# Optimization experiments

Hardware: AMD Instinct MI355X
Metric: run time of the kernel (lower is better)

## Reference

```python
import jax, jax.numpy as jnp
import numpy as np
import math

NEG = -1000000.0

def setup_inputs() -> dict:
    key = jax.random.key(0)
    k1, k2, k3, k4 = jax.random.split(key, 4)
    B, S, D = 64, 1024, 64
    query = jax.random.normal(k1, (B, S, D), dtype=jnp.float32)
    key_t = jax.random.normal(k2, (B, S, D), dtype=jnp.float32)
    value = jax.random.normal(k3, (B, S, D), dtype=jnp.float32)
    valid_lens = jax.random.randint(k4, (B,), 1, S + 1, dtype=jnp.int32)
    return {"query": query, "key": key_t, "value": value, "valid_lens": valid_lens}

def reference(query, key, value, valid_lens):
    # query/key/value: [B, S, D]; valid_lens: [B]
    d = query.shape[-1]
    scores = jnp.einsum('bqd,bkd->bqk', query, key) / math.sqrt(d)
    Sk = key.shape[1]
    # 1D valid_lens -> same mask for every query row (repeat_interleave semantics)
    mask = jnp.arange(Sk)[None, None, :] < valid_lens[:, None, None]  # [B,1,Sk]
    scores = jnp.where(mask, scores, NEG)
    weights = jax.nn.softmax(scores, axis=-1)
    # dropout p=0.0 -> identity
    return jnp.einsum('bqk,bkd->bqd', weights, value)
```

## Files before the change

### kernel.cpp

```cpp
#include <hip/hip_runtime.h>
#include <hip/hip_bf16.h>
#include <cstdint>


typedef __attribute__((ext_vector_type(8))) short short8;
typedef __attribute__((ext_vector_type(4))) short short4v;
typedef __attribute__((ext_vector_type(4))) float f32x4;

#define B_   64
#define S_   1024
#define D_   64
#define BQ   64
#define BK   64
#define KPAD 68

__device__ __forceinline__ uint32_t pk2(float a, float b) {
    float2 t; t.x = a; t.y = b;
    union { __hip_bfloat162 h; uint32_t u; } c;
    c.h = __float22bfloat162_rn(t);
    return c.u;
}
__device__ __forceinline__ unsigned short pbf(float f) {
    union { float f; uint32_t u; } v; v.f = f;
    return (unsigned short)((v.u + 0x8000u) >> 16);
}
__device__ __forceinline__ short8 ld8(const unsigned short* p) {
    short4v lo = *(const short4v*)p;
    short4v hi = *(const short4v*)(p + 4);
    return __builtin_shufflevector(lo, hi, 0, 1, 2, 3, 4, 5, 6, 7);
}

__global__ __launch_bounds__(256, 4)
void attn_fwd(const float* __restrict__ Q, const float* __restrict__ K,
              const float* __restrict__ V, const int* __restrict__ VL,
              float* __restrict__ Out) {
    __shared__ __align__(16) unsigned short lK [2][BK * KPAD];
    __shared__ __align__(16) unsigned short lVt[2][D_ * 64];
    __shared__ __align__(16) unsigned short lP [4 * 16 * KPAD];

    const int tid  = threadIdx.x;
    const int wave = tid >> 6;
    const int lane = tid & 63;
    const int col  = lane & 15;
    const int quad = lane >> 4;

    const int bid  = blockIdx.x;
    const int b    = (bid & 7) * 8 + (bid >> 7);
    const int q0   = ((bid >> 3) & 15) * BQ;
    const int vlen = VL[b];
    const int ntiles = (vlen + BK - 1) / BK;

    const int T  = tid >> 4;
    const int m  = tid & 15;
    const int Tl = T & 3;
    const int cb = T >> 2;
    const int dcs = m >> 1;
    const int sws = ((dcs & 1) << 2) | (dcs >> 1);

    const float* Kb = K + (size_t)b * S_ * D_ + 4 * m;
    const float* Vb = V + (size_t)b * S_ * D_ + 4 * m;

    float4 kr[4], vr[4];
    {
        #pragma unroll
        for (int j = 0; j < 4; ++j) {
            const int row = 2 * T + (j >> 1) * 32 + (j & 1);
            kr[j] = *(const float4*)(Kb + (size_t)row * D_);
            vr[j] = *(const float4*)(Vb + (size_t)row * D_);
        }
    }

    short8 qa[2];
    {
        const int qrow = q0 + wave * 16 + col;
        const float* qp = Q + ((size_t)b * S_ + qrow) * D_ + quad * 8;
        #pragma unroll
        for (int c = 0; c < 2; ++c) {
            float4 x0 = *(const float4*)(qp + c * 32);
            float4 x1 = *(const float4*)(qp + c * 32 + 4);
            union { uint32_t u[4]; short8 s; } qq;
            qq.u[0] = pk2(x0.x, x0.y);
            qq.u[1] = pk2(x0.z, x0.w);
            qq.u[2] = pk2(x1.x, x1.y);
            qq.u[3] = pk2(x1.z, x1.w);
            qa[c] = qq.s;
        }
    }

    f32x4 ofrag[4];
    #pragma unroll
    for (int dt = 0; dt < 4; ++dt) ofrag[dt] = (f32x4){0.f, 0.f, 0.f, 0.f};
    float lsum[4] = {0.f, 0.f, 0.f, 0.f};

    const float cexp = 0.18033688011112042f;

    for (int kt = 0; kt < ntiles; ++kt) {
        unsigned short* bK = lK[kt & 1];
        unsigned short* bV = lVt[kt & 1];

        #pragma unroll
        for (int j = 0; j < 4; ++j) {
            const int row = 2 * T + (j >> 1) * 32 + (j & 1);
            uint2 kv;
            kv.x = pk2(kr[j].x, kr[j].y);
            kv.y = pk2(kr[j].z, kr[j].w);
            *(uint2*)&bK[row * KPAD + 4 * m] = kv;
        }
        #pragma unroll
        for (int i = 0; i < 2; ++i) {
            const int p = (cb + 4 * i) ^ sws;
            unsigned short* base = &bV[p * 8 + 2 * Tl];
            const float4 va = vr[2 * i], vb2 = vr[2 * i + 1];
            *(uint32_t*)&base[(4 * m + 0) * 64] = pk2(va.x, vb2.x);
            *(uint32_t*)&base[(4 * m + 1) * 64] = pk2(va.y, vb2.y);
            *(uint32_t*)&base[(4 * m + 2) * 64] = pk2(va.z, vb2.z);
            *(uint32_t*)&base[(4 * m + 3) * 64] = pk2(va.w, vb2.w);
        }

        if (kt + 1 < ntiles) {
            const size_t off = (size_t)(kt + 1) * BK * D_;
            #pragma unroll
            for (int j = 0; j < 4; ++j) {
                const int row = 2 * T + (j >> 1) * 32 + (j & 1);
                kr[j] = *(const float4*)(Kb + off + (size_t)row * D_);
                vr[j] = *(const float4*)(Vb + off + (size_t)row * D_);
            }
        }

        __syncthreads();

        const int kbase = kt * BK;
        f32x4 sfrag[4];
        #pragma unroll
        for (int ct = 0; ct < 4; ++ct) {
            f32x4 acc = (f32x4){0.f, 0.f, 0.f, 0.f};
            #pragma unroll
            for (int c = 0; c < 2; ++c) {
                short8 kb2 = ld8(&bK[(ct * 16 + col) * KPAD + c * 32 + quad * 8]);
                acc = __builtin_amdgcn_mfma_f32_16x16x32_bf16(qa[c], kb2, acc, 0, 0, 0);
            }
            sfrag[ct] = acc;
        }

        unsigned short* pw = &lP[wave * 16 * KPAD];
        if (kbase + BK <= vlen) {
            #pragma unroll
            for (int ct = 0; ct < 4; ++ct)
                #pragma unroll
                for (int rr = 0; rr < 4; ++rr) {
                    float e = __builtin_amdgcn_exp2f(sfrag[ct][rr] * cexp);
                    lsum[rr] += e;
                    pw[(quad * 4 + rr) * KPAD + ct * 16 + col] = pbf(e);
                }
        } else {
            #pragma unroll
            for (int ct = 0; ct < 4; ++ct) {
                const bool ok = (kbase + ct * 16 + col) < vlen;
                #pragma unroll
                for (int rr = 0; rr < 4; ++rr) {
                    float e = ok ? __builtin_amdgcn_exp2f(sfrag[ct][rr] * cexp) : 0.0f;
                    lsum[rr] += e;
                    pw[(quad * 4 + rr) * KPAD + ct * 16 + col] = pbf(e);
                }
            }
        }

        #pragma unroll
        for (int kc = 0; kc < 2; ++kc) {
            short8 pa = ld8(&pw[col * KPAD + kc * 32 + quad * 8]);
            #pragma unroll
            for (int dt = 0; dt < 4; ++dt) {
                const int sr = ((col >> 3) << 2) | dt;
                const int p  = (kc * 4 + quad) ^ sr;
                short8 vb = *(const short8*)&bV[(dt * 16 + col) * 64 + p * 8];
                ofrag[dt] = __builtin_amdgcn_mfma_f32_16x16x32_bf16(pa, vb, ofrag[dt], 0, 0, 0);
            }
        }
    }

    float inv[4];
    #pragma unroll
    for (int rr = 0; rr < 4; ++rr) {
        float s = lsum[rr];
        #pragma unroll
        for (int mm = 1; mm < 16; mm <<= 1) s += __shfl_xor(s, mm, 64);
        inv[rr] = 1.0f / s;
    }
    const int qrow0 = q0 + wave * 16 + quad * 4;
    #pragma unroll
    for (int rr = 0; rr < 4; ++rr) {
        float* op = Out + ((size_t)b * S_ + qrow0 + rr) * D_ + col;
        #pragma unroll
        for (int dt = 0; dt < 4; ++dt)
            op[dt * 16] = ofrag[dt][rr] * inv[rr];
    }
}

extern "C" void kernel_launch(void* const* d_in, const int* in_sizes, int n_in,
                              void* d_out, int out_size, void* d_ws, size_t ws_size,
                              hipStream_t stream) {
    const float* Q  = (const float*)d_in[0];
    const float* K  = (const float*)d_in[1];
    const float* V  = (const float*)d_in[2];
    const int*   VL = (const int*)d_in[3];
    float* Out = (float*)d_out;
    dim3 grid(B_ * (S_ / BQ));
    attn_fwd<<<grid, 256, 0, stream>>>(Q, K, V, VL, Out);
}
```

Measured before the change: 118.1 us.

## Transpose QK MFMA operands to write packed P rows and single-buffer LDS

The QK^T MFMA now takes K as the A operand and Q as B, so each lane holds four consecutive key scores for one query row. P can then be stored as packed bf16 uint2 writes instead of scalar stores, and row sums collapse to one scalar per lane, reduced with two cross-quad shuffles. KPAD goes from 68 to 72 so that 16-byte LDS reads are aligned, and the K/V LDS buffers drop from double to single buffering, with an extra barrier per tile. This cuts LDS store count and shrinks LDS use, which may improve occupancy, at the cost of one more __syncthreads per iteration.

```diff
diff --git a/kernel.cpp b/kernel.cpp
--- a/kernel.cpp
+++ b/kernel.cpp
@@ -4,7 +4,6 @@
 
 
 typedef __attribute__((ext_vector_type(8))) short short8;
-typedef __attribute__((ext_vector_type(4))) short short4v;
 typedef __attribute__((ext_vector_type(4))) float f32x4;
 
 #define B_   64
@@ -12,7 +11,7 @@
 #define D_   64
 #define BQ   64
 #define BK   64
-#define KPAD 68
+#define KPAD 72
 
 __device__ __forceinline__ uint32_t pk2(float a, float b) {
     float2 t; t.x = a; t.y = b;
@@ -20,22 +19,13 @@
     c.h = __float22bfloat162_rn(t);
     return c.u;
 }
-__device__ __forceinline__ unsigned short pbf(float f) {
-    union { float f; uint32_t u; } v; v.f = f;
-    return (unsigned short)((v.u + 0x8000u) >> 16);
-}
-__device__ __forceinline__ short8 ld8(const unsigned short* p) {
-    short4v lo = *(const short4v*)p;
-    short4v hi = *(const short4v*)(p + 4);
-    return __builtin_shufflevector(lo, hi, 0, 1, 2, 3, 4, 5, 6, 7);
-}
 
 __global__ __launch_bounds__(256, 4)
 void attn_fwd(const float* __restrict__ Q, const float* __restrict__ K,
               const float* __restrict__ V, const int* __restrict__ VL,
               float* __restrict__ Out) {
-    __shared__ __align__(16) unsigned short lK [2][BK * KPAD];
-    __shared__ __align__(16) unsigned short lVt[2][D_ * 64];
+    __shared__ __align__(16) unsigned short lK [BK * KPAD];
+    __shared__ __align__(16) unsigned short lVt[D_ * 64];
     __shared__ __align__(16) unsigned short lP [4 * 16 * KPAD];
 
     const int tid  = threadIdx.x;
@@ -61,13 +51,11 @@
     const float* Vb = V + (size_t)b * S_ * D_ + 4 * m;
 
     float4 kr[4], vr[4];
-    {
-        #pragma unroll
-        for (int j = 0; j < 4; ++j) {
-            const int row = 2 * T + (j >> 1) * 32 + (j & 1);
-            kr[j] = *(const float4*)(Kb + (size_t)row * D_);
-            vr[j] = *(const float4*)(Vb + (size_t)row * D_);
-        }
+    #pragma unroll
+    for (int j = 0; j < 4; ++j) {
+        const int row = 2 * T + (j >> 1) * 32 + (j & 1);
+        kr[j] = *(const float4*)(Kb + (size_t)row * D_);
+        vr[j] = *(const float4*)(Vb + (size_t)row * D_);
     }
 
     short8 qa[2];
@@ -90,13 +78,15 @@
     f32x4 ofrag[4];
     #pragma unroll
     for (int dt = 0; dt < 4; ++dt) ofrag[dt] = (f32x4){0.f, 0.f, 0.f, 0.f};
-    float lsum[4] = {0.f, 0.f, 0.f, 0.f};
+    float lsum = 0.f;
 
     const float cexp = 0.18033688011112042f;
+    unsigned short* pw = &lP[wave * 16 * KPAD];
 
     for (int kt = 0; kt < ntiles; ++kt) {
-        unsigned short* bK = lK[kt & 1];
-        unsigned short* bV = lVt[kt & 1];
+        const int kbase = kt * BK;
+
+        __syncthreads();
 
         #pragma unroll
         for (int j = 0; j < 4; ++j) {
@@ -104,12 +94,12 @@
             uint2 kv;
             kv.x = pk2(kr[j].x, kr[j].y);
             kv.y = pk2(kr[j].z, kr[j].w);
-            *(uint2*)&bK[row * KPAD + 4 * m] = kv;
+            *(uint2*)&lK[row * KPAD + 4 * m] = kv;
         }
         #pragma unroll
         for (int i = 0; i < 2; ++i) {
             const int p = (cb + 4 * i) ^ sws;
-            unsigned short* base = &bV[p * 8 + 2 * Tl];
+            unsigned short* base = &lVt[p * 8 + 2 * Tl];
             const float4 va = vr[2 * i], vb2 = vr[2 * i + 1];
             *(uint32_t*)&base[(4 * m + 0) * 64] = pk2(va.x, vb2.x);
             *(uint32_t*)&base[(4 * m + 1) * 64] = pk2(va.y, vb2.y);
@@ -129,70 +119,69 @@
 
         __syncthreads();
 
-        const int kbase = kt * BK;
         f32x4 sfrag[4];
         #pragma unroll
         for (int ct = 0; ct < 4; ++ct) {
             f32x4 acc = (f32x4){0.f, 0.f, 0.f, 0.f};
             #pragma unroll
             for (int c = 0; c < 2; ++c) {
-                short8 kb2 = ld8(&bK[(ct * 16 + col) * KPAD + c * 32 + quad * 8]);
-                acc = __builtin_amdgcn_mfma_f32_16x16x32_bf16(qa[c], kb2, acc, 0, 0, 0);
+                short8 kf = *(const short8*)&lK[(ct * 16 + col) * KPAD + c * 32 + quad * 8];
+                acc = __builtin_amdgcn_mfma_f32_16x16x32_bf16(kf, qa[c], acc, 0, 0, 0);
             }
             sfrag[ct] = acc;
         }
 
-        unsigned short* pw = &lP[wave * 16 * KPAD];
         if (kbase + BK <= vlen) {
             #pragma unroll
-            for (int ct = 0; ct < 4; ++ct)
-                #pragma unroll
-                for (int rr = 0; rr < 4; ++rr) {
-                    float e = __builtin_amdgcn_exp2f(sfrag[ct][rr] * cexp);
-                    lsum[rr] += e;
-                    pw[(quad * 4 + rr) * KPAD + ct * 16 + col] = pbf(e);
-                }
+            for (int ct = 0; ct < 4; ++ct) {
+                float e0 = __builtin_amdgcn_exp2f(sfrag[ct][0] * cexp);
+                float e1 = __builtin_amdgcn_exp2f(sfrag[ct][1] * cexp);
+                float e2 = __builtin_amdgcn_exp2f(sfrag[ct][2] * cexp);
+                float e3 = __builtin_amdgcn_exp2f(sfrag[ct][3] * cexp);
+                lsum += (e0 + e1) + (e2 + e3);
+                uint2 pk; pk.x = pk2(e0, e1); pk.y = pk2(e2, e3);
+                *(uint2*)&pw[col * KPAD + ct * 16 + quad * 4] = pk;
+            }
         } else {
             #pragma unroll
             for (int ct = 0; ct < 4; ++ct) {
-                const bool ok = (kbase + ct * 16 + col) < vlen;
+                const int kv0 = kbase + ct * 16 + quad * 4;
+                float e[4];
                 #pragma unroll
                 for (int rr = 0; rr < 4; ++rr) {
-                    float e = ok ? __builtin_amdgcn_exp2f(sfrag[ct][rr] * cexp) : 0.0f;
-                    lsum[rr] += e;
-                    pw[(quad * 4 + rr) * KPAD + ct * 16 + col] = pbf(e);
+                    e[rr] = (kv0 + rr < vlen)
+                          ? __builtin_amdgcn_exp2f(sfrag[ct][rr] * cexp) : 0.0f;
+                    lsum += e[rr];
                 }
+                uint2 pk; pk.x = pk2(e[0], e[1]); pk.y = pk2(e[2], e[3]);
+                *(uint2*)&pw[col * KPAD + ct * 16 + quad * 4] = pk;
             }
         }
 
         #pragma unroll
         for (int kc = 0; kc < 2; ++kc) {
-            short8 pa = ld8(&pw[col * KPAD + kc * 32 + quad * 8]);
+            short8 pa = *(const short8*)&pw[col * KPAD + kc * 32 + quad * 8];
             #pragma unroll
             for (int dt = 0; dt < 4; ++dt) {
                 const int sr = ((col >> 3) << 2) | dt;
                 const int p  = (kc * 4 + quad) ^ sr;
-                short8 vb = *(const short8*)&bV[(dt * 16 + col) * 64 + p * 8];
+                short8 vb = *(const short8*)&lVt[(dt * 16 + col) * 64 + p * 8];
                 ofrag[dt] = __builtin_amdgcn_mfma_f32_16x16x32_bf16(pa, vb, ofrag[dt], 0, 0, 0);
             }
         }
     }
 
-    float inv[4];
-    #pragma unroll
-    for (int rr = 0; rr < 4; ++rr) {
-        float s = lsum[rr];
-        #pragma unroll
-        for (int mm = 1; mm < 16; mm <<= 1) s += __shfl_xor(s, mm, 64);
-        inv[rr] = 1.0f / s;
-    }
+    float s = lsum;
+    s += __shfl_xor(s, 16, 64);
+    s += __shfl_xor(s, 32, 64);
     const int qrow0 = q0 + wave * 16 + quad * 4;
     #pragma unroll
     for (int rr = 0; rr < 4; ++rr) {
+        const float inv = 1.0f / __shfl(s, quad * 4 + rr, 64);
         float* op = Out + ((size_t)b * S_ + qrow0 + rr) * D_ + col;
         #pragma unroll
         for (int dt = 0; dt < 4; ++dt)
-            op[dt * 16] = ofrag[dt][rr] * inv[rr];
+            op[dt * 16] = ofrag[dt][rr] * inv;
     }
 }
 
```

Result: faster. 115.0 us (-2.6%).
